# Optimization experiments

Measured on AMD Instinct MI355X. Metric: run time of the kernel, lower is better.

Reference implementation:

```python
import math
import jax, jax.numpy as jnp
import numpy as np

B, C, H, W = 8, 512, 32, 32
HEADS = 8


def _mix_rot(re, im, Wm, phi):
    # nn.Linear(dim, dim, bias=False) applied channelwise on [B,C,H,W]:
    # y = x @ Wm.T  ->  einsum over input channel c, output channel d
    re2 = jnp.einsum('bchw,dc->bdhw', re, Wm)
    im2 = jnp.einsum('bchw,dc->bdhw', im, Wm)
    c = jnp.cos(phi)[None, :, None, None]
    s = jnp.sin(phi)[None, :, None, None]
    # complex multiply (re2 + i*im2) * (cos phi + i*sin phi)
    return re2 * c - im2 * s, re2 * s + im2 * c


def setup_inputs() -> dict:
    key = jax.random.key(0)
    ks = jax.random.split(key, 6)
    scale = 1.0 / math.sqrt(C)
    return {
        'z_re': jax.random.normal(ks[0], (B, C, H, W), jnp.float32),
        'z_im': jax.random.normal(ks[1], (B, C, H, W), jnp.float32),
        'Wq': jax.random.normal(ks[2], (C, C), jnp.float32) * scale,
        'phi_q': jnp.zeros((C,), jnp.float32),
        'Wk': jax.random.normal(ks[3], (C, C), jnp.float32) * scale,
        'phi_k': jnp.zeros((C,), jnp.float32),
        'Wv': jax.random.normal(ks[4], (C, C), jnp.float32) * scale,
        'phi_v': jnp.zeros((C,), jnp.float32),
        'Wo': jax.random.normal(ks[5], (C, C), jnp.float32) * scale,
        'phi_o': jnp.zeros((C,), jnp.float32),
    }


def reference(z_re, z_im, Wq, phi_q, Wk, phi_k, Wv, phi_v, Wo, phi_o):
    b, c, h, w = z_re.shape
    T = h * w
    dh = c // HEADS

    def tok(a):  # [B,C,H,W] -> [B,T,C]
        return a.reshape(b, c, T).transpose(0, 2, 1)

    qre, qim = _mix_rot(z_re, z_im, Wq, phi_q)
    kre, kim = _mix_rot(z_re, z_im, Wk, phi_k)
    vre, vim = _mix_rot(z_re, z_im, Wv, phi_v)
    qre, qim = tok(qre), tok(qim)
    kre, kim = tok(kre), tok(kim)
    vre, vim = tok(vre), tok(vim)

    # real part of complex inner product: sums over FULL channel dim (no head split)
    scores = (jnp.einsum('btc,buc->btu', qre, kre)
              + jnp.einsum('btc,buc->btu', qim, kim)) / math.sqrt(dh)
    causal = jnp.triu(jnp.ones((T, T), bool), k=1)
    scores = jnp.where(causal[None], -jnp.inf, scores)
    attn = jax.nn.softmax(scores, axis=-1)

    out_re = jnp.einsum('btu,buc->btc', attn, vre)
    out_im = jnp.einsum('btu,buc->btc', attn, vim)

    def grid(a):  # [B,T,C] -> [B,C,H,W]
        return a.transpose(0, 2, 1).reshape(b, c, h, w)

    return _mix_rot(grid(out_re), grid(out_im), Wo, phi_o)
```

## Files before the change

kernel.cpp:

```cpp
#include <hip/hip_runtime.h>
#include <math.h>

#define NB 8
#define NC 512
#define NT 1024
#define BT (NB * NT)
#define SCALE 0.125f
#define NEG_BIG (-3.0e38f)

typedef __attribute__((ext_vector_type(8))) short short8v;
typedef __attribute__((ext_vector_type(8))) _Float16 half8v;
typedef __attribute__((ext_vector_type(4))) float float4v;
#define MFMA_BF16(A, B, C) __builtin_amdgcn_mfma_f32_16x16x32_bf16(A, B, C, 0, 0, 0)
#define MFMA_F16(A, B, C)  __builtin_amdgcn_mfma_f32_16x16x32_f16(A, B, C, 0, 0, 0)

__device__ __forceinline__ ushort f2bf(float f) {
    union { float f; unsigned int i; } v; v.f = f;
    unsigned int r = v.i + 0x7FFFu + ((v.i >> 16) & 1u);
    return (ushort)(r >> 16);
}

__device__ __forceinline__ ushort f2h(float f) {
    return __builtin_bit_cast(unsigned short, (_Float16)f);
}

__device__ __forceinline__ half8v scale8(short8v raw, float s) {
    half8v h = __builtin_bit_cast(half8v, raw);
    const _Float16 hs = (_Float16)s;
    half8v r;
    #pragma unroll
    for (int q = 0; q < 8; ++q) r[q] = h[q] * hs;
    return r;
}

#if defined(__has_builtin)
#if __has_builtin(__builtin_amdgcn_global_load_lds)
#define HAS_GLDS 1
#endif
#endif

#ifdef HAS_GLDS
__device__ __forceinline__ void glds16(const ushort* g, ushort* l) {
    __builtin_amdgcn_global_load_lds(
        (const __attribute__((address_space(1))) unsigned int*)g,
        (__attribute__((address_space(3))) unsigned int*)l, 16, 0, 0);
}
#endif

template<int ROWS>
__device__ __forceinline__ void stage64(const ushort* __restrict__ g, int rsShorts,
                                        ushort* tile, int w, int lane) {
    const int r8 = lane >> 3;
    const int ck = (lane & 7) ^ r8;
    const ushort* gl = g + (size_t)r8 * rsShorts + (ck << 3);
    constexpr int ni = ROWS / 32;
    #pragma unroll
    for (int s = 0; s < ni; ++s) {
        const int issue = w * ni + s;
#ifdef HAS_GLDS
        glds16(gl + (size_t)issue * 8 * rsShorts, tile + issue * 512);
#else
        const uint4 v = *(const uint4*)(gl + (size_t)issue * 8 * rsShorts);
        *(uint4*)(tile + issue * 512 + lane * 8) = v;
#endif
    }
}

__device__ __forceinline__ short8v frag(const ushort* tile, int rr, int q) {
    return *(const short8v*)(tile + rr * 64 + ((q ^ (rr & 7)) << 3));
}

__global__ __launch_bounds__(256) void prep_z_kernel(
    const float* __restrict__ zre, const float* __restrict__ zim,
    ushort* __restrict__ Z)
{
    const int t0 = blockIdx.x << 6, c0 = blockIdx.y << 6;
    const int bz = blockIdx.z, b = bz & 7, comp = bz >> 3;
    const float* src = (comp ? zim : zre) + (size_t)b * NC * NT;
    ushort* dst = Z + (size_t)(comp * NB + b) * NT * NC;
    const int tid = threadIdx.x;

    __shared__ ushort T[64][72];
    #pragma unroll
    for (int r = 0; r < 4; ++r) {
        const int cl = (tid >> 4) + r * 16;
        const int t4 = (tid & 15) << 2;
        const float4 v = *(const float4*)(src + (size_t)(c0 + cl) * NT + t0 + t4);
        T[t4 + 0][cl] = f2bf(v.x); T[t4 + 1][cl] = f2bf(v.y);
        T[t4 + 2][cl] = f2bf(v.z); T[t4 + 3][cl] = f2bf(v.w);
    }
    __syncthreads();
    const int tl = tid >> 2, cc = (tid & 3) << 4;
    ushort* op = dst + (size_t)(t0 + tl) * NC + c0 + cc;
    *(uint4*)op       = *(const uint4*)&T[tl][cc];
    *(uint4*)(op + 8) = *(const uint4*)&T[tl][cc + 8];
}

__global__ __launch_bounds__(256) void prep_w_kernel(
    const float* __restrict__ Wq, const float* __restrict__ Wk,
    const float* __restrict__ Wv, const float* __restrict__ Wo,
    ushort* __restrict__ Wbf)
{
    const int idx = blockIdx.x * 256 + threadIdx.x;
    const int e4 = idx << 2;
    const int m = e4 >> 18;
    const int off = e4 & ((1 << 18) - 1);
    const float* Ws[4] = {Wq, Wk, Wv, Wo};
    const float4 v = *(const float4*)(Ws[m] + off);
    ushort4 o;
    o.x = f2bf(v.x); o.y = f2bf(v.y); o.z = f2bf(v.z); o.w = f2bf(v.w);
    *(ushort4*)(Wbf + ((size_t)m << 18) + off) = o;
}

__global__ __launch_bounds__(256, 2) void proj_qk_kernel(
    const ushort* __restrict__ Z, const ushort* __restrict__ Wbf,
    const float* __restrict__ phiq, const float* __restrict__ phik,
    ushort* __restrict__ qre, ushort* __restrict__ qim,
    ushort* __restrict__ kre, ushort* __restrict__ kim)
{
    const int tid = threadIdx.x;
    const int m0 = blockIdx.x << 7;
    const int d0 = blockIdx.y << 6;
    const size_t NE = (size_t)BT * NC;

    __shared__ alignas(16) ushort Zr[128 * 64], Zi[128 * 64];
    __shared__ alignas(16) ushort Wq_s[64 * 64], Wk_s[64 * 64];

    float4v accq[2][4][2] = {};
    float4v acck[2][4][2] = {};

    const int w = tid >> 6, lane = tid & 63;
    const int l15 = lane & 15, quad = lane >> 4;
    const int wm = (w & 1) << 6;
    const int wn = (w >> 1) << 5;

    for (int c0 = 0; c0 < NC; c0 += 64) {
        stage64<128>(Z + (size_t)m0 * NC + c0, NC, Zr, w, lane);
        stage64<128>(Z + NE + (size_t)m0 * NC + c0, NC, Zi, w, lane);
        stage64<64>(Wbf + (size_t)d0 * NC + c0, NC, Wq_s, w, lane);
        stage64<64>(Wbf + ((size_t)1 << 18) + (size_t)d0 * NC + c0, NC, Wk_s, w, lane);
        __syncthreads();
        #pragma unroll
        for (int kk = 0; kk < 2; ++kk) {
            const int q0 = kk * 4 + quad;
            short8v zf[2][4], wqf[2], wkf[2];
            #pragma unroll
            for (int i = 0; i < 4; ++i) {
                zf[0][i] = frag(Zr, wm + i * 16 + l15, q0);
                zf[1][i] = frag(Zi, wm + i * 16 + l15, q0);
            }
            #pragma unroll
            for (int j = 0; j < 2; ++j) {
                wqf[j] = frag(Wq_s, wn + j * 16 + l15, q0);
                wkf[j] = frag(Wk_s, wn + j * 16 + l15, q0);
            }
            #pragma unroll
            for (int c = 0; c < 2; ++c)
                #pragma unroll
                for (int i = 0; i < 4; ++i)
                    #pragma unroll
                    for (int j = 0; j < 2; ++j) {
                        accq[c][i][j] = MFMA_BF16(zf[c][i], wqf[j], accq[c][i][j]);
                        acck[c][i][j] = MFMA_BF16(zf[c][i], wkf[j], acck[c][i][j]);
                    }
        }
        __syncthreads();
    }

    #pragma unroll
    for (int j = 0; j < 2; ++j) {
        const int d = d0 + wn + j * 16 + l15;
        const float pq = phiq[d], pk = phik[d];
        const float cq = cosf(pq), sq = sinf(pq);
        const float ck = cosf(pk), sk = sinf(pk);
        #pragma unroll
        for (int i = 0; i < 4; ++i)
            #pragma unroll
            for (int r = 0; r < 4; ++r) {
                const size_t m = m0 + wm + i * 16 + quad * 4 + r;
                const size_t off = m * NC + d;
                const float ar = accq[0][i][j][r], ai = accq[1][i][j][r];
                qre[off] = f2bf(ar * cq - ai * sq);
                qim[off] = f2bf(ar * sq + ai * cq);
                const float br = acck[0][i][j][r], bi = acck[1][i][j][r];
                kre[off] = f2bf(br * ck - bi * sk);
                kim[off] = f2bf(br * sk + bi * ck);
            }
    }
}

__global__ __launch_bounds__(256, 3) void proj_v_kernel(
    const ushort* __restrict__ Z, const ushort* __restrict__ Wbf,
    const float* __restrict__ phiv,
    ushort* __restrict__ vre, ushort* __restrict__ vim)
{
    const int tid = threadIdx.x;
    const int d0 = blockIdx.x << 7;
    const int bt0 = blockIdx.y << 6;
    const size_t NE = (size_t)BT * NC;

    __shared__ alignas(16) ushort Wv_s[128 * 64], Zr[64 * 64], Zi[64 * 64];
    float4v acc[2][4][2] = {};

    const int w = tid >> 6, lane = tid & 63;
    const int l15 = lane & 15, quad = lane >> 4;
    const int wm = (w & 1) << 6;
    const int wn = (w >> 1) << 5;

    for (int c0 = 0; c0 < NC; c0 += 64) {
        stage64<128>(Wbf + ((size_t)2 << 18) + (size_t)d0 * NC + c0, NC, Wv_s, w, lane);
        stage64<64>(Z + (size_t)bt0 * NC + c0, NC, Zr, w, lane);
        stage64<64>(Z + NE + (size_t)bt0 * NC + c0, NC, Zi, w, lane);
        __syncthreads();
        #pragma unroll
        for (int kk = 0; kk < 2; ++kk) {
            const int q0 = kk * 4 + quad;
            short8v wvf[4], zf[2][2];
            #pragma unroll
            for (int i = 0; i < 4; ++i)
                wvf[i] = frag(Wv_s, wm + i * 16 + l15, q0);
            #pragma unroll
            for (int j = 0; j < 2; ++j) {
                zf[0][j] = frag(Zr, wn + j * 16 + l15, q0);
                zf[1][j] = frag(Zi, wn + j * 16 + l15, q0);
            }
            #pragma unroll
            for (int c = 0; c < 2; ++c)
                #pragma unroll
                for (int i = 0; i < 4; ++i)
                    #pragma unroll
                    for (int j = 0; j < 2; ++j)
                        acc[c][i][j] = MFMA_BF16(wvf[i], zf[c][j], acc[c][i][j]);
        }
        __syncthreads();
    }

    #pragma unroll
    for (int i = 0; i < 4; ++i)
        #pragma unroll
        for (int r = 0; r < 4; ++r) {
            const int d = d0 + wm + i * 16 + quad * 4 + r;
            const float ph = phiv[d];
            const float cs = cosf(ph), sn = sinf(ph);
            #pragma unroll
            for (int j = 0; j < 2; ++j) {
                const int bt = bt0 + wn + j * 16 + l15;
                const int b = bt >> 10, t = bt & 1023;
                const size_t off = (size_t)b * NC * NT + (size_t)d * NT + t;
                const float vr = acc[0][i][j][r], vi = acc[1][i][j][r];
                vre[off] = f2h(vr * cs - vi * sn);
                vim[off] = f2h(vr * sn + vi * cs);
            }
        }
}

__global__ __launch_bounds__(256, 3) void scores_kernel(
    const ushort* __restrict__ qre, const ushort* __restrict__ qim,
    const ushort* __restrict__ kre, const ushort* __restrict__ kim,
    ushort* __restrict__ Pp, float2* __restrict__ stats)
{
    const int u0b = blockIdx.x << 7;
    const int t0b = (gridDim.y - 1 - blockIdx.y) << 7;
    if (u0b > t0b) return;
    const int b = blockIdx.z;
    const int tid = threadIdx.x;
    const size_t qb = (size_t)b * NT * NC;

    __shared__ alignas(16) ushort Qr[128 * 64], Qi[128 * 64], Kr[128 * 64], Ki[128 * 64];
    float4v acc[4][4] = {};

    const int w = tid >> 6, lane = tid & 63;
    const int l15 = lane & 15, quad = lane >> 4;
    const int wm = (w & 1) << 6;
    const int wn = (w >> 1) << 6;

    for (int c0 = 0; c0 < NC; c0 += 64) {
        stage64<128>(qre + qb + (size_t)t0b * NC + c0, NC, Qr, w, lane);
        stage64<128>(qim + qb + (size_t)t0b * NC + c0, NC, Qi, w, lane);
        stage64<128>(kre + qb + (size_t)u0b * NC + c0, NC, Kr, w, lane);
        stage64<128>(kim + qb + (size_t)u0b * NC + c0, NC, Ki, w, lane);
        __syncthreads();
        #pragma unroll
        for (int kk = 0; kk < 2; ++kk) {
            const int q0 = kk * 4 + quad;
            short8v qf[2][4], kf[2][4];
            #pragma unroll
            for (int i = 0; i < 4; ++i) {
                qf[0][i] = frag(Qr, wm + i * 16 + l15, q0);
                qf[1][i] = frag(Qi, wm + i * 16 + l15, q0);
                kf[0][i] = frag(Kr, wn + i * 16 + l15, q0);
                kf[1][i] = frag(Ki, wn + i * 16 + l15, q0);
            }
            #pragma unroll
            for (int i = 0; i < 4; ++i)
                #pragma unroll
                for (int j = 0; j < 4; ++j) {
                    acc[i][j] = MFMA_BF16(qf[0][i], kf[0][j], acc[i][j]);
                    acc[i][j] = MFMA_BF16(qf[1][i], kf[1][j], acc[i][j]);
                }
        }
        __syncthreads();
    }

    const int sub = (u0b + wn) >> 6;
    float2* st = stats + (size_t)(b * 16 + sub) * NT;
    ushort* Pb = Pp + (size_t)b * NT * NT;
    #pragma unroll
    for (int i = 0; i < 4; ++i)
        #pragma unroll
        for (int r = 0; r < 4; ++r) {
            const int t = t0b + wm + i * 16 + quad * 4 + r;
            float v[4]; float m = NEG_BIG;
            #pragma unroll
            for (int j = 0; j < 4; ++j) {
                const int u = u0b + wn + j * 16 + l15;
                const float x = (u > t) ? NEG_BIG : acc[i][j][r] * SCALE;
                v[j] = x; m = fmaxf(m, x);
            }
            #pragma unroll
            for (int d = 1; d < 16; d <<= 1) m = fmaxf(m, __shfl_xor(m, d, 64));
            float l = 0.f; ushort ph[4];
            #pragma unroll
            for (int j = 0; j < 4; ++j) {
                const float e = __expf(v[j] - m);
                l += e;
                ph[j] = f2h(e);
            }
            #pragma unroll
            for (int d = 1; d < 16; d <<= 1) l += __shfl_xor(l, d, 64);
            ushort* pr = Pb + (size_t)t * NT + u0b + wn + l15;
            #pragma unroll
            for (int j = 0; j < 4; ++j) pr[j * 16] = ph[j];
            if (l15 == 0) st[t] = make_float2(m, l);
        }
}

__global__ __launch_bounds__(256, 3) void pv_kernel(
    const ushort* __restrict__ Pp, const float2* __restrict__ stats,
    const ushort* __restrict__ vre, const ushort* __restrict__ vim,
    ushort* __restrict__ Ore, ushort* __restrict__ Oim)
{
    const int c0b = blockIdx.x << 6;
    const int t0b = (gridDim.y - 1 - blockIdx.y) << 7;
    const int b = blockIdx.z;
    const int tid = threadIdx.x;
    const ushort* P = Pp + ((size_t)b * NT + t0b) * NT;
    const size_t vb = (size_t)b * NC * NT;
    const int iters = (t0b + 128) >> 6;

    __shared__ alignas(16) ushort Ps[128 * 64], Vr[64 * 64], Vi[64 * 64];
    __shared__ float sLds[128][17];
    float4v acc[2][4][2] = {};

    const int w = tid >> 6, lane = tid & 63;
    const int l15 = lane & 15, quad = lane >> 4;
    const int wm = (w & 1) << 6;
    const int wn = (w >> 1) << 5;

    if (tid < 128) {
        const int t = t0b + tid;
        float M = NEG_BIG;
        for (int s = 0; s < iters; ++s)
            M = fmaxf(M, stats[(size_t)(b * 16 + s) * NT + t].x);
        float L = 0.f;
        for (int s = 0; s < iters; ++s) {
            const float2 v = stats[(size_t)(b * 16 + s) * NT + t];
            const float e = __expf(v.x - M);
            sLds[tid][s] = e;
            L += e * v.y;
        }
        const float inv = 1.0f / L;
        for (int s = 0; s < iters; ++s) sLds[tid][s] *= inv;
    }

    for (int it = 0; it < iters; ++it) {
        const int u0 = it << 6;
        stage64<128>(P + u0, NT, Ps, w, lane);
        stage64<64>(vre + vb + (size_t)c0b * NT + u0, NT, Vr, w, lane);
        stage64<64>(vim + vb + (size_t)c0b * NT + u0, NT, Vi, w, lane);
        __syncthreads();
        #pragma unroll
        for (int kk = 0; kk < 2; ++kk) {
            const int q0 = kk * 4 + quad;
            half8v pf[4], vf[2][2];
            #pragma unroll
            for (int i = 0; i < 4; ++i) {
                const int row = wm + i * 16 + l15;
                pf[i] = scale8(frag(Ps, row, q0), sLds[row][it]);
            }
            #pragma unroll
            for (int j = 0; j < 2; ++j) {
                vf[0][j] = __builtin_bit_cast(half8v, frag(Vr, wn + j * 16 + l15, q0));
                vf[1][j] = __builtin_bit_cast(half8v, frag(Vi, wn + j * 16 + l15, q0));
            }
            #pragma unroll
            for (int c = 0; c < 2; ++c)
                #pragma unroll
                for (int i = 0; i < 4; ++i)
                    #pragma unroll
                    for (int j = 0; j < 2; ++j)
                        acc[c][i][j] = MFMA_F16(pf[i], vf[c][j], acc[c][i][j]);
        }
        __syncthreads();
    }
    #pragma unroll
    for (int i = 0; i < 4; ++i)
        #pragma unroll
        for (int j = 0; j < 2; ++j)
            #pragma unroll
            for (int r = 0; r < 4; ++r) {
                const int t = t0b + wm + i * 16 + quad * 4 + r;
                const int c = c0b + wn + j * 16 + l15;
                const size_t off = ((size_t)b * NT + t) * NC + c;
                Ore[off] = f2bf(acc[0][i][j][r]);
                Oim[off] = f2bf(acc[1][i][j][r]);
            }
}

__global__ __launch_bounds__(256, 3) void proj_out_kernel(
    const ushort* __restrict__ Ore, const ushort* __restrict__ Oim,
    const ushort* __restrict__ Wbf, const float* __restrict__ phio,
    float* __restrict__ outRe, float* __restrict__ outIm)
{
    const int tid = threadIdx.x;
    const int d0 = blockIdx.x << 7;
    const int bt0 = blockIdx.y << 6;

    __shared__ alignas(16) ushort Wo_s[128 * 64], Or_s[64 * 64], Oi_s[64 * 64];
    float4v acc[2][4][2] = {};

    const int w = tid >> 6, lane = tid & 63;
    const int l15 = lane & 15, quad = lane >> 4;
    const int wm = (w & 1) << 6;
    const int wn = (w >> 1) << 5;

    for (int c0 = 0; c0 < NC; c0 += 64) {
        stage64<128>(Wbf + ((size_t)3 << 18) + (size_t)d0 * NC + c0, NC, Wo_s, w, lane);
        stage64<64>(Ore + (size_t)bt0 * NC + c0, NC, Or_s, w, lane);
        stage64<64>(Oim + (size_t)bt0 * NC + c0, NC, Oi_s, w, lane);
        __syncthreads();
        #pragma unroll
        for (int kk = 0; kk < 2; ++kk) {
            const int q0 = kk * 4 + quad;
            short8v wof[4], of[2][2];
            #pragma unroll
            for (int i = 0; i < 4; ++i)
                wof[i] = frag(Wo_s, wm + i * 16 + l15, q0);
            #pragma unroll
            for (int j = 0; j < 2; ++j) {
                of[0][j] = frag(Or_s, wn + j * 16 + l15, q0);
                of[1][j] = frag(Oi_s, wn + j * 16 + l15, q0);
            }
            #pragma unroll
            for (int c = 0; c < 2; ++c)
                #pragma unroll
                for (int i = 0; i < 4; ++i)
                    #pragma unroll
                    for (int j = 0; j < 2; ++j)
                        acc[c][i][j] = MFMA_BF16(wof[i], of[c][j], acc[c][i][j]);
        }
        __syncthreads();
    }

    #pragma unroll
    for (int i = 0; i < 4; ++i)
        #pragma unroll
        for (int r = 0; r < 4; ++r) {
            const int d = d0 + wm + i * 16 + quad * 4 + r;
            const float ph = phio[d];
            const float cs = cosf(ph), sn = sinf(ph);
            #pragma unroll
            for (int j = 0; j < 2; ++j) {
                const int bt = bt0 + wn + j * 16 + l15;
                const int b = bt >> 10, t = bt & 1023;
                const size_t off = (size_t)b * NC * NT + (size_t)d * NT + t;
                const float re2 = acc[0][i][j][r], im2 = acc[1][i][j][r];
                outRe[off] = re2 * cs - im2 * sn;
                outIm[off] = re2 * sn + im2 * cs;
            }
        }
}

extern "C" void kernel_launch(void* const* d_in, const int* in_sizes, int n_in,
                              void* d_out, int out_size, void* d_ws, size_t ws_size,
                              hipStream_t stream) {
    (void)in_sizes; (void)n_in; (void)out_size; (void)ws_size;
    const float* z_re  = (const float*)d_in[0];
    const float* z_im  = (const float*)d_in[1];
    const float* Wq    = (const float*)d_in[2];
    const float* phi_q = (const float*)d_in[3];
    const float* Wk    = (const float*)d_in[4];
    const float* phi_k = (const float*)d_in[5];
    const float* Wv    = (const float*)d_in[6];
    const float* phi_v = (const float*)d_in[7];
    const float* Wo    = (const float*)d_in[8];
    const float* phi_o = (const float*)d_in[9];

    const size_t NE = (size_t)BT * NC;
    ushort* ws  = (ushort*)d_ws;
    ushort* qre = ws + 0 * NE; ushort* qim = ws + 1 * NE;
    ushort* kre = ws + 2 * NE; ushort* kim = ws + 3 * NE;
    ushort* vre = ws + 4 * NE; ushort* vim = ws + 5 * NE;
    ushort* Wbf = ws + 6 * NE;
    ushort* Z  = (ushort*)d_out;
    ushort* Pp = (ushort*)d_out + 2 * NE;
    float2* stats = (float2*)d_out;

    const dim3 blk(256);
    hipLaunchKernelGGL(prep_z_kernel, dim3(NT / 64, NC / 64, NB * 2), blk, 0, stream, z_re, z_im, Z);
    hipLaunchKernelGGL(prep_w_kernel, dim3(1024), blk, 0, stream, Wq, Wk, Wv, Wo, Wbf);
    hipLaunchKernelGGL(proj_qk_kernel, dim3(BT / 128, NC / 64), blk, 0, stream,
                       Z, Wbf, phi_q, phi_k, qre, qim, kre, kim);
    hipLaunchKernelGGL(proj_v_kernel, dim3(NC / 128, BT / 64), blk, 0, stream,
                       Z, Wbf, phi_v, vre, vim);
    hipLaunchKernelGGL(scores_kernel, dim3(NT / 128, NT / 128, NB), blk, 0, stream,
                       qre, qim, kre, kim, Pp, stats);
    hipLaunchKernelGGL(pv_kernel, dim3(NC / 64, NT / 128, NB), blk, 0, stream,
                       Pp, stats, vre, vim, qre, qim);
    hipLaunchKernelGGL(proj_out_kernel, dim3(NC / 128, BT / 64), blk, 0, stream,
                       qre, qim, Wbf, phi_o, (float*)d_out, (float*)d_out + NE);
}
```

Baseline: 233.9 us.

## Stage kernel epilogues through LDS for coalesced vectorized global stores

Every GEMM-style kernel (QK projection, V projection, scores, PV, output projection) now writes its MFMA accumulator tile into a padded shared-memory buffer that aliases the staging buffers. It then reads the tile back row-contiguously and issues 8- or 16-byte vector stores in place of scattered 2- or 4-byte stores. The phase sin/cos values are computed once per lane and broadcast with wave shuffles, and the pv stats reduction is fully unrolled into registers. This targets uncoalesced write traffic at the cost of extra barriers and LDS round-trips.

```diff
diff --git a/kernel.cpp b/kernel.cpp
--- a/kernel.cpp
+++ b/kernel.cpp
@@ -123,8 +123,12 @@
     const int d0 = blockIdx.y << 6;
     const size_t NE = (size_t)BT * NC;
 
-    __shared__ alignas(16) ushort Zr[128 * 64], Zi[128 * 64];
-    __shared__ alignas(16) ushort Wq_s[64 * 64], Wk_s[64 * 64];
+    __shared__ alignas(16) ushort SM[24576];
+    ushort* Zr   = SM;
+    ushort* Zi   = SM + 8192;
+    ushort* Wq_s = SM + 16384;
+    ushort* Wk_s = SM + 20480;
+    uint*   R    = (uint*)SM;
 
     float4v accq[2][4][2] = {};
     float4v acck[2][4][2] = {};
@@ -167,25 +171,69 @@
         __syncthreads();
     }
 
+    float cq[2], sq[2], ck2[2], sk2[2];
     #pragma unroll
     for (int j = 0; j < 2; ++j) {
         const int d = d0 + wn + j * 16 + l15;
         const float pq = phiq[d], pk = phik[d];
-        const float cq = cosf(pq), sq = sinf(pq);
-        const float ck = cosf(pk), sk = sinf(pk);
+        cq[j] = cosf(pq); sq[j] = sinf(pq);
+        ck2[j] = cosf(pk); sk2[j] = sinf(pk);
+    }
+    const int g = tid >> 4, cl = tid & 15;
+
+    #pragma unroll
+    for (int j = 0; j < 2; ++j)
         #pragma unroll
         for (int i = 0; i < 4; ++i)
             #pragma unroll
             for (int r = 0; r < 4; ++r) {
-                const size_t m = m0 + wm + i * 16 + quad * 4 + r;
-                const size_t off = m * NC + d;
+                const int row = wm + i * 16 + quad * 4 + r;
+                const int col = wn + j * 16 + l15;
                 const float ar = accq[0][i][j][r], ai = accq[1][i][j][r];
-                qre[off] = f2bf(ar * cq - ai * sq);
-                qim[off] = f2bf(ar * sq + ai * cq);
+                R[row * 76 + col] = (uint)f2bf(ar * cq[j] - ai * sq[j])
+                                  | ((uint)f2bf(ar * sq[j] + ai * cq[j]) << 16);
+            }
+    __syncthreads();
+    #pragma unroll
+    for (int s = 0; s < 8; ++s) {
+        const int row = g * 8 + s;
+        const uint4 p = *(const uint4*)&R[row * 76 + cl * 4];
+        uint2 re, im;
+        re.x = (p.x & 0xFFFFu) | (p.y << 16);
+        re.y = (p.z & 0xFFFFu) | (p.w << 16);
+        im.x = (p.x >> 16) | (p.y & 0xFFFF0000u);
+        im.y = (p.z >> 16) | (p.w & 0xFFFF0000u);
+        const size_t off = (size_t)(m0 + row) * NC + d0 + cl * 4;
+        *(uint2*)(qre + off) = re;
+        *(uint2*)(qim + off) = im;
+    }
+    __syncthreads();
+
+    #pragma unroll
+    for (int j = 0; j < 2; ++j)
+        #pragma unroll
+        for (int i = 0; i < 4; ++i)
+            #pragma unroll
+            for (int r = 0; r < 4; ++r) {
+                const int row = wm + i * 16 + quad * 4 + r;
+                const int col = wn + j * 16 + l15;
                 const float br = acck[0][i][j][r], bi = acck[1][i][j][r];
-                kre[off] = f2bf(br * ck - bi * sk);
-                kim[off] = f2bf(br * sk + bi * ck);
-            }
+                R[row * 76 + col] = (uint)f2bf(br * ck2[j] - bi * sk2[j])
+                                  | ((uint)f2bf(br * sk2[j] + bi * ck2[j]) << 16);
+            }
+    __syncthreads();
+    #pragma unroll
+    for (int s = 0; s < 8; ++s) {
+        const int row = g * 8 + s;
+        const uint4 p = *(const uint4*)&R[row * 76 + cl * 4];
+        uint2 re, im;
+        re.x = (p.x & 0xFFFFu) | (p.y << 16);
+        re.y = (p.z & 0xFFFFu) | (p.w << 16);
+        im.x = (p.x >> 16) | (p.y & 0xFFFF0000u);
+        im.y = (p.z >> 16) | (p.w & 0xFFFF0000u);
+        const size_t off = (size_t)(m0 + row) * NC + d0 + cl * 4;
+        *(uint2*)(kre + off) = re;
+        *(uint2*)(kim + off) = im;
     }
 }
 
@@ -199,7 +247,12 @@
     const int bt0 = blockIdx.y << 6;
     const size_t NE = (size_t)BT * NC;
 
-    __shared__ alignas(16) ushort Wv_s[128 * 64], Zr[64 * 64], Zi[64 * 64];
+    __shared__ alignas(16) ushort SM[19456];
+    ushort* Wv_s = SM;
+    ushort* Zr   = SM + 8192;
+    ushort* Zi   = SM + 12288;
+    uint*   R    = (uint*)SM;
+
     float4v acc[2][4][2] = {};
 
     const int w = tid >> 6, lane = tid & 63;
@@ -235,23 +288,42 @@
         __syncthreads();
     }
 
+    const int d_own = d0 + wm + (l15 >> 2) * 16 + quad * 4 + (l15 & 3);
+    const float ph_own = phiv[d_own];
+    const float c_own = cosf(ph_own), s_own = sinf(ph_own);
+
     #pragma unroll
     for (int i = 0; i < 4; ++i)
         #pragma unroll
         for (int r = 0; r < 4; ++r) {
-            const int d = d0 + wm + i * 16 + quad * 4 + r;
-            const float ph = phiv[d];
-            const float cs = cosf(ph), sn = sinf(ph);
+            const int src = (lane & 48) | (i * 4 + r);
+            const float cs = __shfl(c_own, src, 64);
+            const float sn = __shfl(s_own, src, 64);
+            const int row = wm + i * 16 + quad * 4 + r;
             #pragma unroll
             for (int j = 0; j < 2; ++j) {
-                const int bt = bt0 + wn + j * 16 + l15;
-                const int b = bt >> 10, t = bt & 1023;
-                const size_t off = (size_t)b * NC * NT + (size_t)d * NT + t;
+                const int col = wn + j * 16 + l15;
                 const float vr = acc[0][i][j][r], vi = acc[1][i][j][r];
-                vre[off] = f2h(vr * cs - vi * sn);
-                vim[off] = f2h(vr * sn + vi * cs);
-            }
-        }
+                R[row * 76 + col] = (uint)f2h(vr * cs - vi * sn)
+                                  | ((uint)f2h(vr * sn + vi * cs) << 16);
+            }
+        }
+    __syncthreads();
+    const int g = tid >> 4, cl = tid & 15;
+    const int b = bt0 >> 10, t0 = bt0 & 1023;
+    #pragma unroll
+    for (int s = 0; s < 8; ++s) {
+        const int row = g * 8 + s;
+        const uint4 p = *(const uint4*)&R[row * 76 + cl * 4];
+        uint2 re, im;
+        re.x = (p.x & 0xFFFFu) | (p.y << 16);
+        re.y = (p.z & 0xFFFFu) | (p.w << 16);
+        im.x = (p.x >> 16) | (p.y & 0xFFFF0000u);
+        im.y = (p.z >> 16) | (p.w & 0xFFFF0000u);
+        const size_t off = (size_t)b * NC * NT + (size_t)(d0 + row) * NT + t0 + cl * 4;
+        *(uint2*)(vre + off) = re;
+        *(uint2*)(vim + off) = im;
+    }
 }
 
 __global__ __launch_bounds__(256, 3) void scores_kernel(
@@ -266,7 +338,13 @@
     const int tid = threadIdx.x;
     const size_t qb = (size_t)b * NT * NC;
 
-    __shared__ alignas(16) ushort Qr[128 * 64], Qi[128 * 64], Kr[128 * 64], Ki[128 * 64];
+    __shared__ alignas(16) ushort SM[32768];
+    ushort* Qr = SM;
+    ushort* Qi = SM + 8192;
+    ushort* Kr = SM + 16384;
+    ushort* Ki = SM + 24576;
+    ushort* Rs = SM;
+
     float4v acc[4][4] = {};
 
     const int w = tid >> 6, lane = tid & 63;
@@ -304,7 +382,6 @@
 
     const int sub = (u0b + wn) >> 6;
     float2* st = stats + (size_t)(b * 16 + sub) * NT;
-    ushort* Pb = Pp + (size_t)b * NT * NT;
     #pragma unroll
     for (int i = 0; i < 4; ++i)
         #pragma unroll
@@ -319,20 +396,27 @@
             }
             #pragma unroll
             for (int d = 1; d < 16; d <<= 1) m = fmaxf(m, __shfl_xor(m, d, 64));
-            float l = 0.f; ushort ph[4];
+            float l = 0.f;
+            const int row = wm + i * 16 + quad * 4 + r;
             #pragma unroll
             for (int j = 0; j < 4; ++j) {
                 const float e = __expf(v[j] - m);
                 l += e;
-                ph[j] = f2h(e);
+                Rs[row * 140 + wn + j * 16 + l15] = f2h(e);
             }
             #pragma unroll
             for (int d = 1; d < 16; d <<= 1) l += __shfl_xor(l, d, 64);
-            ushort* pr = Pb + (size_t)t * NT + u0b + wn + l15;
-            #pragma unroll
-            for (int j = 0; j < 4; ++j) pr[j * 16] = ph[j];
             if (l15 == 0) st[t] = make_float2(m, l);
         }
+    __syncthreads();
+    ushort* Pb = Pp + (size_t)b * NT * NT;
+    const int g = tid >> 5, cl = tid & 31;
+    #pragma unroll
+    for (int s = 0; s < 16; ++s) {
+        const int row = g * 16 + s;
+        const uint2 p = *(const uint2*)&Rs[row * 140 + cl * 4];
+        *(uint2*)(Pb + (size_t)(t0b + row) * NT + u0b + cl * 4) = p;
+    }
 }
 
 __global__ __launch_bounds__(256, 3) void pv_kernel(
@@ -348,8 +432,13 @@
     const size_t vb = (size_t)b * NC * NT;
     const int iters = (t0b + 128) >> 6;
 
-    __shared__ alignas(16) ushort Ps[128 * 64], Vr[64 * 64], Vi[64 * 64];
-    __shared__ float sLds[128][17];
+    __shared__ alignas(16) ushort SM[20736];
+    ushort* Ps = SM;
+    ushort* Vr = SM + 8192;
+    ushort* Vi = SM + 12288;
+    float* sLds = (float*)(SM + 16384);
+    uint*  R    = (uint*)SM;
+
     float4v acc[2][4][2] = {};
 
     const int w = tid >> 6, lane = tid & 63;
@@ -359,18 +448,23 @@
 
     if (tid < 128) {
         const int t = t0b + tid;
+        float mv[16], lv[16];
+        #pragma unroll
+        for (int s = 0; s < 16; ++s) {
+            if (s < iters) {
+                const float2 v = stats[(size_t)(b * 16 + s) * NT + t];
+                mv[s] = v.x; lv[s] = v.y;
+            } else { mv[s] = NEG_BIG; lv[s] = 0.f; }
+        }
         float M = NEG_BIG;
-        for (int s = 0; s < iters; ++s)
-            M = fmaxf(M, stats[(size_t)(b * 16 + s) * NT + t].x);
-        float L = 0.f;
-        for (int s = 0; s < iters; ++s) {
-            const float2 v = stats[(size_t)(b * 16 + s) * NT + t];
-            const float e = __expf(v.x - M);
-            sLds[tid][s] = e;
-            L += e * v.y;
-        }
+        #pragma unroll
+        for (int s = 0; s < 16; ++s) M = fmaxf(M, mv[s]);
+        float L = 0.f; float ev[16];
+        #pragma unroll
+        for (int s = 0; s < 16; ++s) { ev[s] = __expf(mv[s] - M); L += ev[s] * lv[s]; }
         const float inv = 1.0f / L;
-        for (int s = 0; s < iters; ++s) sLds[tid][s] *= inv;
+        #pragma unroll
+        for (int s = 0; s < 16; ++s) sLds[tid * 17 + s] = ev[s] * inv;
     }
 
     for (int it = 0; it < iters; ++it) {
@@ -386,7 +480,7 @@
             #pragma unroll
             for (int i = 0; i < 4; ++i) {
                 const int row = wm + i * 16 + l15;
-                pf[i] = scale8(frag(Ps, row, q0), sLds[row][it]);
+                pf[i] = scale8(frag(Ps, row, q0), sLds[row * 17 + it]);
             }
             #pragma unroll
             for (int j = 0; j < 2; ++j) {
@@ -403,18 +497,33 @@
         }
         __syncthreads();
     }
+
     #pragma unroll
     for (int i = 0; i < 4; ++i)
         #pragma unroll
         for (int j = 0; j < 2; ++j)
             #pragma unroll
             for (int r = 0; r < 4; ++r) {
-                const int t = t0b + wm + i * 16 + quad * 4 + r;
-                const int c = c0b + wn + j * 16 + l15;
-                const size_t off = ((size_t)b * NT + t) * NC + c;
-                Ore[off] = f2bf(acc[0][i][j][r]);
-                Oim[off] = f2bf(acc[1][i][j][r]);
-            }
+                const int row = wm + i * 16 + quad * 4 + r;
+                const int col = wn + j * 16 + l15;
+                R[row * 76 + col] = (uint)f2bf(acc[0][i][j][r])
+                                  | ((uint)f2bf(acc[1][i][j][r]) << 16);
+            }
+    __syncthreads();
+    const int g = tid >> 4, cl = tid & 15;
+    #pragma unroll
+    for (int s = 0; s < 8; ++s) {
+        const int row = g * 8 + s;
+        const uint4 p = *(const uint4*)&R[row * 76 + cl * 4];
+        uint2 re, im;
+        re.x = (p.x & 0xFFFFu) | (p.y << 16);
+        re.y = (p.z & 0xFFFFu) | (p.w << 16);
+        im.x = (p.x >> 16) | (p.y & 0xFFFF0000u);
+        im.y = (p.z >> 16) | (p.w & 0xFFFF0000u);
+        const size_t off = ((size_t)b * NT + t0b + row) * NC + c0b + cl * 4;
+        *(uint2*)(Ore + off) = re;
+        *(uint2*)(Oim + off) = im;
+    }
 }
 
 __global__ __launch_bounds__(256, 3) void proj_out_kernel(
@@ -426,7 +535,12 @@
     const int d0 = blockIdx.x << 7;
     const int bt0 = blockIdx.y << 6;
 
-    __shared__ alignas(16) ushort Wo_s[128 * 64], Or_s[64 * 64], Oi_s[64 * 64];
+    __shared__ alignas(16) ushort SM[19456];
+    ushort* Wo_s = SM;
+    ushort* Or_s = SM + 8192;
+    ushort* Oi_s = SM + 12288;
+    float*  Rf   = (float*)SM;
+
     float4v acc[2][4][2] = {};
 
     const int w = tid >> 6, lane = tid & 63;
@@ -462,23 +576,56 @@
         __syncthreads();
     }
 
+    const int d_own = d0 + wm + (l15 >> 2) * 16 + quad * 4 + (l15 & 3);
+    const float ph_own = phio[d_own];
+    const float c_own = cosf(ph_own), s_own = sinf(ph_own);
+    const int g = tid >> 4, cl = tid & 15;
+    const int b = bt0 >> 10, t0 = bt0 & 1023;
+
     #pragma unroll
     for (int i = 0; i < 4; ++i)
         #pragma unroll
         for (int r = 0; r < 4; ++r) {
-            const int d = d0 + wm + i * 16 + quad * 4 + r;
-            const float ph = phio[d];
-            const float cs = cosf(ph), sn = sinf(ph);
+            const int src = (lane & 48) | (i * 4 + r);
+            const float cs = __shfl(c_own, src, 64);
+            const float sn = __shfl(s_own, src, 64);
+            const int row = wm + i * 16 + quad * 4 + r;
             #pragma unroll
             for (int j = 0; j < 2; ++j) {
-                const int bt = bt0 + wn + j * 16 + l15;
-                const int b = bt >> 10, t = bt & 1023;
-                const size_t off = (size_t)b * NC * NT + (size_t)d * NT + t;
-                const float re2 = acc[0][i][j][r], im2 = acc[1][i][j][r];
-                outRe[off] = re2 * cs - im2 * sn;
-                outIm[off] = re2 * sn + im2 * cs;
-            }
-        }
+                const int col = wn + j * 16 + l15;
+                Rf[row * 76 + col] = acc[0][i][j][r] * cs - acc[1][i][j][r] * sn;
+            }
+        }
+    __syncthreads();
+    #pragma unroll
+    for (int s = 0; s < 8; ++s) {
+        const int row = g * 8 + s;
+        const float4 p = *(const float4*)&Rf[row * 76 + cl * 4];
+        *(float4*)(outRe + (size_t)b * NC * NT + (size_t)(d0 + row) * NT + t0 + cl * 4) = p;
+    }
+    __syncthreads();
+
+    #pragma unroll
+    for (int i = 0; i < 4; ++i)
+        #pragma unroll
+        for (int r = 0; r < 4; ++r) {
+            const int src = (lane & 48) | (i * 4 + r);
+            const float cs = __shfl(c_own, src, 64);
+            const float sn = __shfl(s_own, src, 64);
+            const int row = wm + i * 16 + quad * 4 + r;
+            #pragma unroll
+            for (int j = 0; j < 2; ++j) {
+                const int col = wn + j * 16 + l15;
+                Rf[row * 76 + col] = acc[0][i][j][r] * sn + acc[1][i][j][r] * cs;
+            }
+        }
+    __syncthreads();
+    #pragma unroll
+    for (int s = 0; s < 8; ++s) {
+        const int row = g * 8 + s;
+        const float4 p = *(const float4*)&Rf[row * 76 + cl * 4];
+        *(float4*)(outIm + (size_t)b * NC * NT + (size_t)(d0 + row) * NT + t0 + cl * 4) = p;
+    }
 }
 
 extern "C" void kernel_launch(void* const* d_in, const int* in_sizes, int n_in,
```

New measurement: 210.8 us. 1.11x faster.
